# Kernel optimization log

Hardware: AMD Instinct MI355X
Metric: run time of the kernel (lower is better)

## Reference

```python
import jax, jax.numpy as jnp
import numpy as np

NE, NR = 100000, 200
STT, ABS, REL, RDIM = 512, 256, 256, 384
GAMMA = 12.0
PI = 3.141592653589793
EMB_RNG_R = float(np.sqrt(6.0 / (NR + RDIM)))
B = 8192


def setup_inputs() -> dict:
    key = jax.random.key(0)
    ks = jax.random.split(key, 16)
    cols = [
        jax.random.randint(ks[0], (B, 1), 0, NE),      # s
        jax.random.randint(ks[1], (B, 1), 0, NR),      # r
        jax.random.randint(ks[2], (B, 1), 0, NE),      # o
        jax.random.randint(ks[3], (B, 1), 0, 31),      # d
        jax.random.randint(ks[4], (B, 1), 0, 12),      # m
        jax.random.randint(ks[5], (B, 1), 0, 100),     # y
        jax.random.randint(ks[6], (B, 2 * NR), 0, 1000),  # context times
    ]
    x = jnp.concatenate(cols, axis=1).astype(jnp.int64)
    s = 0.02
    return {
        "x": x,
        "e_emb": jax.random.normal(ks[7], (NE, STT), jnp.float32) * s,
        "r_emb": jax.random.normal(ks[8], (NR, RDIM), jnp.float32) * s,
        "d_frq": jax.random.normal(ks[9], (NE, ABS), jnp.float32) * s,
        "d_phi": jax.random.normal(ks[10], (NE, ABS), jnp.float32) * s,
        "d_amp": jax.random.normal(ks[11], (NE, ABS // 2), jnp.float32) * s,
        "m_frq": jax.random.normal(ks[12], (NE, ABS), jnp.float32) * s,
        "m_phi": jax.random.normal(ks[13], (NE, ABS), jnp.float32) * s,
        "m_amp": jax.random.normal(ks[14], (NE, ABS // 2), jnp.float32) * s,
        "w_e": jax.random.normal(ks[15], (STT, REL // 2), jnp.float32) * s,
        "w_rp": jax.random.normal(jax.random.fold_in(key, 99), (NR, NR, 1), jnp.float32) * s,
    }


def _pos_emb(t):  # t: float [N] -> [N, REL]
    f = 1.0 / (10000.0 ** (jnp.arange(0, REL, 2, dtype=jnp.float32) / REL))
    rs = t[:, None] * f[None, :]
    return jnp.concatenate([jnp.cos(rs), jnp.sin(rs)], axis=1)


def reference(x, e_emb, r_emb, d_frq, d_phi, d_amp, m_frq, m_phi, m_amp, w_e, w_rp):
    f32 = jnp.float32

    def t_emb(e, d, m):  # e int [B], d,m float [B,1] -> [B, ABS]
        re_d, im_d = jnp.split(d * d_frq[e] + d_phi[e], 2, axis=1)
        ad = d_amp[e]
        demb = jnp.concatenate([ad * jnp.cos(re_d), ad * jnp.sin(im_d)], axis=1)
        re_m, im_m = jnp.split(m * m_frq[e] + m_phi[e], 2, axis=1)
        am = m_amp[e]
        memb = jnp.concatenate([am * jnp.cos(re_m), am * jnp.sin(im_m)], axis=1)
        return demb + memb

    def e_p_emb(e):  # e: [B,1,STT] -> [B,1,REL]
        re_w, im_w = jnp.split(w_e, 2, axis=0)
        re_e, im_e = jnp.split(e, 2, axis=2)
        re_p = re_e @ re_w - im_e @ im_w
        im_p = im_e @ re_w - re_e @ im_w  # note: minus, matching source
        return jnp.concatenate([re_p, im_p], axis=2)

    def e_r_emb(r_idx, e_t):  # e_t: [B,NR] float -> [B,REL,1]
        er = _pos_emb(e_t.reshape(-1)).reshape(e_t.shape[0], NR, REL)
        er = jnp.transpose(er, (0, 2, 1))  # [B,REL,NR]
        return jnp.einsum('bdn,bno->bdo', er, w_rp[r_idx])

    s_idx, r_idx, o_idx = x[:, 0], x[:, 1], x[:, 2]
    d_abs = x[:, 3:4].astype(f32)
    m_abs = x[:, 4:5].astype(f32)
    c_s = x[:, -2 * NR:-NR].astype(f32)
    c_o = x[:, -NR:].astype(f32)

    s = e_emb[s_idx][:, None, :]
    s_t = t_emb(s_idx, d_abs, m_abs)[:, None, :]
    s_p = e_p_emb(s)
    s_r = e_r_emb(r_idx, c_s)

    o = e_emb[o_idx][:, None, :]
    o_t = t_emb(o_idx, d_abs, m_abs)[:, None, :]
    o_p = e_p_emb(o)
    o_r = e_r_emb(r_idx, c_o)

    r = r_emb[r_idx][:, None, :]  # [B,1,RDIM]
    p_r = r / (EMB_RNG_R / PI)
    re_r, im_r = jnp.cos(p_r), jnp.sin(p_r)

    re_s, im_s = jnp.split(s, 2, axis=2)
    re_st, im_st = jnp.split(s_t, 2, axis=2)
    re_s = jnp.concatenate([re_s, re_st], axis=2)  # [B,1,RDIM]
    im_s = jnp.concatenate([im_s, im_st], axis=2)
    re_o, im_o = jnp.split(o, 2, axis=2)
    re_ot, im_ot = jnp.split(o_t, 2, axis=2)
    re_o = jnp.concatenate([re_o, re_ot], axis=2)
    im_o = jnp.concatenate([im_o, im_ot], axis=2)

    # RotatE complex rotation score on static+absolute part
    re_sc = re_s * re_r - im_s * im_r - re_o
    im_sc = re_s * im_r + im_s * re_r - im_o
    sc_abs = jnp.sqrt(re_sc * re_sc + im_sc * im_sc).sum(axis=2)

    # relative-time score from projected embeddings + relation-context embeddings
    s_rel = s_p + jnp.transpose(s_r, (0, 2, 1))  # [B,1,REL]
    o_rel = o_p + jnp.transpose(o_r, (0, 2, 1))
    re_sr, im_sr = jnp.split(s_rel, 2, axis=2)
    re_or, im_or = jnp.split(o_rel, 2, axis=2)
    dre, dim = re_sr - re_or, im_sr - im_or
    sc_rel = jnp.sqrt(dre * dre + dim * dim).sum(axis=2)

    return GAMMA - (sc_abs + sc_rel)  # [B,1]
```

## Files before the change

### kernel.cpp

```cpp
#include <hip/hip_runtime.h>
#include <cstdint>

#define B_ROWS 8192
#define XSTR   406
#define GAMMA_C 12.0f
#define SCALE_ANG 30.994217f

#define KH     1024
#define HPAD   1028

#define NT_BLK 128
#define NW_BLK 64
#define NF_BLK 512
#define NS_BLK 4096
#define NMRG   (NF_BLK + NS_BLK)

#define TF_BYTES    (KH*256*2)
#define WCAT_BYTES  (512*256*2)
#define WS_FULL     ((size_t)(TF_BYTES + WCAT_BYTES))
#define OLDTAB_BYTES (1000*256*2)
#define WS_OLD       ((size_t)(OLDTAB_BYTES + WCAT_BYTES))

typedef __attribute__((ext_vector_type(8))) short short8v;
typedef __attribute__((ext_vector_type(4))) float float4v;

__device__ __forceinline__ float bfLo(uint32_t u) { return __uint_as_float(u << 16); }
__device__ __forceinline__ float bfHi(uint32_t u) { return __uint_as_float(u & 0xffff0000u); }
__device__ __forceinline__ float bf1(unsigned short u) { return __uint_as_float((uint32_t)u << 16); }

__device__ __forceinline__ uint32_t f2bf_u(float x) {
  uint32_t u = __float_as_uint(x);
  u += 0x7fffu + ((u >> 16) & 1u);
  return u >> 16;
}
__device__ __forceinline__ unsigned short f2bf(float x) { return (unsigned short)f2bf_u(x); }

__device__ __forceinline__ short8v cvt8(float4 a, float4 b) {
  short8v r;
  r[0] = (short)f2bf(a.x); r[1] = (short)f2bf(a.y);
  r[2] = (short)f2bf(a.z); r[3] = (short)f2bf(a.w);
  r[4] = (short)f2bf(b.x); r[5] = (short)f2bf(b.y);
  r[6] = (short)f2bf(b.z); r[7] = (short)f2bf(b.w);
  return r;
}

__global__ __launch_bounds__(256) void kge_prep0(
    const float* __restrict__ w_e,
    unsigned short* __restrict__ tf, unsigned short* __restrict__ wcat) {
  const int bid = blockIdx.x;
  const int tid = threadIdx.x;
  const int sub = tid >> 6, l = tid & 63;
  if (bid < NT_BLK) {
    const int fragid = bid * 4 + sub;
    const int kt = fragid >> 4, nt = fragid & 15;
    const int c = nt * 16 + (l & 15);
    const float f = exp2f(-(float)(c & 127) * (13.287712379549449f / 128.f));
    __align__(16) unsigned short v[8];
    #pragma unroll
    for (int jj = 0; jj < 8; ++jj) {
      int k = kt * 32 + ((l >> 4) << 3) + jj;
      float val = 0.f;
      if (k < 1000) {
        float s, cv;
        sincosf((float)k * f, &s, &cv);
        val = (c < 128) ? cv : s;
      }
      v[jj] = f2bf(val);
    }
    ((uint4*)tf)[fragid * 64 + l] = *(const uint4*)v;
  } else {
    const int fragid = (bid - NT_BLK) * 4 + sub;
    const int kk = fragid >> 4, nt = fragid & 15;
    const int c = nt * 16 + (l & 15);
    __align__(16) unsigned short v[8];
    #pragma unroll
    for (int jj = 0; jj < 8; ++jj) {
      int k = kk * 32 + ((l >> 4) << 3) + jj;
      float s = (k < 256) ? 1.f : -1.f;
      float val = (c < 128) ? s * w_e[k * 128 + c]
                            : -s * w_e[(k ^ 256) * 128 + (c - 128)];
      v[jj] = f2bf(val);
    }
    ((uint4*)wcat)[fragid * 64 + l] = *(const uint4*)v;
  }
}

__global__ __launch_bounds__(256) void kge_merged(
    const int* __restrict__ x, const float* __restrict__ e_emb,
    const float* __restrict__ r_emb,
    const float* __restrict__ d_frq, const float* __restrict__ d_phi, const float* __restrict__ d_amp,
    const float* __restrict__ m_frq, const float* __restrict__ m_phi, const float* __restrict__ m_amp,
    const float* __restrict__ w_rp,
    const unsigned short* __restrict__ wcat, const unsigned short* __restrict__ tf,
    float* __restrict__ out) {
  __shared__ __align__(16) float lds_f[16 * HPAD];
  __shared__ float st2[2][2][256];
  __shared__ float redl[4];
  __shared__ float prel[4][16];
  const int tid = threadIdx.x;
  const int w = tid >> 6, l = tid & 63;

  if (blockIdx.x < NF_BLK) {
    const int m0 = blockIdx.x * 16;

    #pragma unroll
    for (int i = tid; i < 16 * HPAD / 4; i += 256)
      ((float4*)lds_f)[i] = (float4){0, 0, 0, 0};
    __syncthreads();

    {
      const int hr = tid >> 4, sub16 = tid & 15;
      const int row = m0 + hr;
      const int* xr = x + (size_t)row * XSTR;
      const int rid = xr[1];
      const int* cp = xr + 6;
      const float* wp = w_rp + (size_t)rid * 200;
      float* hrow = lds_f + hr * HPAD;
      for (int n = sub16; n < 200; n += 16) {
        float wv = wp[n];
        atomicAdd(&hrow[cp[n]], wv);
        atomicAdd(&hrow[cp[200 + n]], -wv);
      }
    }

    const int rowA = m0 + (l & 15);
    const int* xrA = x + (size_t)rowA * XSTR;
    const float* Esp = e_emb + (size_t)xrA[0] * 512 + ((l >> 4) << 3);
    const float* Eop = e_emb + (size_t)xrA[2] * 512 + ((l >> 4) << 3);
    const short8v* wq = (const short8v*)wcat;
    const short8v* tq = (const short8v*)tf;

    float4v acc[16];
    #pragma unroll
    for (int i = 0; i < 16; ++i) acc[i] = (float4v){0, 0, 0, 0};

    #pragma unroll
    for (int kt = 4 * w; kt < 4 * w + 4; ++kt) {
      float4 s0 = *(const float4*)(Esp + kt * 32);
      float4 s1 = *(const float4*)(Esp + kt * 32 + 4);
      float4 o0 = *(const float4*)(Eop + kt * 32);
      float4 o1 = *(const float4*)(Eop + kt * 32 + 4);
      float4 d0 = {s0.x - o0.x, s0.y - o0.y, s0.z - o0.z, s0.w - o0.w};
      float4 d1 = {s1.x - o1.x, s1.y - o1.y, s1.z - o1.z, s1.w - o1.w};
      short8v a = cvt8(d0, d1);
      const short8v* bsrc = wq + (size_t)kt * 1024;
      #pragma unroll
      for (int nt = 0; nt < 16; ++nt)
        acc[nt] = __builtin_amdgcn_mfma_f32_16x16x32_bf16(a, bsrc[nt * 64 + l], acc[nt], 0, 0, 0);
    }
    __syncthreads();

    {
      const float* hbase = lds_f + (l & 15) * HPAD + ((l >> 4) << 3);
      #pragma unroll
      for (int g = 8 * w; g < 8 * w + 8; ++g) {
        float4 h0 = *(const float4*)(hbase + g * 32);
        float4 h1 = *(const float4*)(hbase + g * 32 + 4);
        short8v a = cvt8(h0, h1);
        const short8v* bsrc = tq + (size_t)g * 1024;
        #pragma unroll
        for (int nt = 0; nt < 16; ++nt)
          acc[nt] = __builtin_amdgcn_mfma_f32_16x16x32_bf16(a, bsrc[nt * 64 + l], acc[nt], 0, 0, 0);
      }
    }
    __syncthreads();

    float* part = lds_f;
    #pragma unroll
    for (int nt = 0; nt < 16; ++nt)
      #pragma unroll
      for (int q = 0; q < 4; ++q)
        part[((w * 16 + nt) * 256) + q * 64 + l] = acc[nt][q];
    __syncthreads();

    {
      float sq[4] = {0.f, 0.f, 0.f, 0.f};
      #pragma unroll
      for (int pp = 0; pp < 2; ++pp) {
        const int p = 2 * w + pp;
        #pragma unroll
        for (int q = 0; q < 4; ++q) {
          const int idx = q * 64 + l;
          float dre = part[(0 * 16 + p) * 256 + idx] + part[(1 * 16 + p) * 256 + idx]
                    + part[(2 * 16 + p) * 256 + idx] + part[(3 * 16 + p) * 256 + idx];
          float dim = part[(0 * 16 + p + 8) * 256 + idx] + part[(1 * 16 + p + 8) * 256 + idx]
                    + part[(2 * 16 + p + 8) * 256 + idx] + part[(3 * 16 + p + 8) * 256 + idx];
          sq[q] += sqrtf(dre * dre + dim * dim);
        }
      }
      #pragma unroll
      for (int q = 0; q < 4; ++q) {
        float s = sq[q];
        s += __shfl_xor(s, 1); s += __shfl_xor(s, 2);
        s += __shfl_xor(s, 4); s += __shfl_xor(s, 8);
        if ((l & 15) == 0) prel[w][(l >> 4) * 4 + q] = s;
      }
    }
    __syncthreads();
    if (tid < 16) {
      const int r = tid;
      float srel = prel[0][r] + prel[1][r] + prel[2][r] + prel[3][r];
      atomicAdd(&out[m0 + r], -srel);
    }
  } else {
    const int bid = blockIdx.x - NF_BLK;
    const int rsub = tid >> 7;
    const int row = bid * 2 + rsub;
    const int j = tid & 127;
    const int* xr = x + (size_t)row * XSTR;
    const int eS = xr[0], rid = xr[1], eO = xr[2];
    const float dv = (float)xr[3], mv = (float)xr[4];
    const int j2 = 2 * j;
    #pragma unroll
    for (int ent = 0; ent < 2; ++ent) {
      const int e = ent ? eO : eS;
      float2 fd = *(const float2*)&d_frq[(size_t)e * 256 + j2];
      float2 pd = *(const float2*)&d_phi[(size_t)e * 256 + j2];
      float2 fm = *(const float2*)&m_frq[(size_t)e * 256 + j2];
      float2 pm = *(const float2*)&m_phi[(size_t)e * 256 + j2];
      const int ja = j2 & 127;
      float2 ad = *(const float2*)&d_amp[(size_t)e * 128 + ja];
      float2 am = *(const float2*)&m_amp[(size_t)e * 128 + ja];
      float a0 = fmaf(dv, fd.x, pd.x), a1 = fmaf(dv, fd.y, pd.y);
      float b0 = fmaf(mv, fm.x, pm.x), b1 = fmaf(mv, fm.y, pm.y);
      float t0, t1, u0, u1;
      if (j2 < 128) { t0 = __cosf(a0); t1 = __cosf(a1); u0 = __cosf(b0); u1 = __cosf(b1); }
      else          { t0 = __sinf(a0); t1 = __sinf(a1); u0 = __sinf(b0); u1 = __sinf(b1); }
      st2[rsub][ent][j2]     = fmaf(ad.x, t0, am.x * u0);
      st2[rsub][ent][j2 + 1] = fmaf(ad.y, t1, am.y * u1);
    }
    __syncthreads();
    const float* Es = e_emb + (size_t)eS * 512;
    const float* Eo = e_emb + (size_t)eO * 512;
    const float* Rr = r_emb + (size_t)rid * 384;
    float sabs = 0.f;
    #pragma unroll
    for (int t3 = 0; t3 < 3; ++t3) {
      const int u = t3 * 128 + j;
      float ang = Rr[u] * SCALE_ANG;
      float sr = __sinf(ang), cr = __cosf(ang);
      float res, ims, reo, imo;
      if (t3 < 2) {
        res = Es[u]; ims = Es[256 + u];
        reo = Eo[u]; imo = Eo[256 + u];
      } else {
        res = st2[rsub][0][j]; ims = st2[rsub][0][128 + j];
        reo = st2[rsub][1][j]; imo = st2[rsub][1][128 + j];
      }
      float rsc = res * cr - ims * sr - reo;
      float isc = res * sr + ims * cr - imo;
      sabs += sqrtf(rsc * rsc + isc * isc);
    }
    #pragma unroll
    for (int off = 32; off > 0; off >>= 1) sabs += __shfl_down(sabs, off);
    if (l == 0) redl[w] = sabs;
    __syncthreads();
    if (j == 0) atomicAdd(&out[row], GAMMA_C - (redl[2 * rsub] + redl[2 * rsub + 1]));
  }
}

#define NTH    512
#define RPB    8
#define ERB    (2*RPB)
#define APAD   520

__global__ void kge_table_old(unsigned short* __restrict__ tab) {
  int t = blockIdx.x;
  int j = threadIdx.x;
  double f = pow(10000.0, -(double)j / 128.0);
  double ang = (double)t * f;
  int q = j >> 1, lo = j & 1;
  tab[t * 256 + 4 * q + lo]     = f2bf((float)cos(ang));
  tab[t * 256 + 4 * q + 2 + lo] = f2bf((float)sin(ang));
}

__global__ void kge_wcat_old(const float* __restrict__ w_e, unsigned short* __restrict__ wcat) {
  int bid = blockIdx.x;
  int kk = bid >> 4, nt = bid & 15;
  int l = threadIdx.x;
  __align__(16) unsigned short v[8];
  int c = nt * 16 + (l & 15);
  #pragma unroll
  for (int j = 0; j < 8; ++j) {
    int k = kk * 32 + ((l >> 4) << 3) + j;
    float s = (k < 256) ? 1.f : -1.f;
    float val = (c < 128) ? s * w_e[k * 128 + c]
                          : -s * w_e[(k ^ 256) * 128 + (c - 128)];
    v[j] = f2bf(val);
  }
  ((uint4*)wcat)[bid * 64 + l] = *(const uint4*)v;
}

__global__ __launch_bounds__(NTH, 4) void kge_main3(
    const int* __restrict__ x,
    const float* __restrict__ e_emb, const float* __restrict__ r_emb,
    const float* __restrict__ d_frq, const float* __restrict__ d_phi, const float* __restrict__ d_amp,
    const float* __restrict__ m_frq, const float* __restrict__ m_phi, const float* __restrict__ m_amp,
    const float* __restrict__ w_rp,
    const unsigned short* __restrict__ tab, const unsigned short* __restrict__ wcat,
    float* __restrict__ out) {
  __shared__ __align__(16) unsigned short A[ERB][APAD];
  __shared__ __align__(16) unsigned short stb[ERB][256];
  __shared__ __align__(16) float p[ERB][256];
  __shared__ int meta[RPB][6];

  const int tid = threadIdx.x;
  const int base_row = blockIdx.x * RPB;
  const int w = tid >> 6, l = tid & 63;

  if (tid < RPB * 6) {
    int r = tid / 6, f = tid % 6;
    meta[r][f] = x[(size_t)(base_row + r) * XSTR + f];
  }
  __syncthreads();

  for (int i = tid; i < ERB * 128; i += NTH) {
    int er = i >> 7, k4 = i & 127;
    int e = (er & 1) ? meta[er >> 1][2] : meta[er >> 1][0];
    float4 v = ((const float4*)e_emb)[(size_t)e * 128 + k4];
    uint2 pk;
    pk.x = f2bf_u(v.x) | (f2bf_u(v.y) << 16);
    pk.y = f2bf_u(v.z) | (f2bf_u(v.w) << 16);
    *(uint2*)&A[er][k4 * 4] = pk;
  }
  for (int it = tid; it < ERB * 256; it += NTH) {
    int j = it & 255, er = it >> 8, r = er >> 1;
    int e = (er & 1) ? meta[r][2] : meta[r][0];
    float dv = (float)meta[r][3], mv = (float)meta[r][4];
    size_t b256 = (size_t)e * 256 + j, b128 = (size_t)e * 128 + (j & 127);
    float argd = fmaf(dv, d_frq[b256], d_phi[b256]);
    float argm = fmaf(mv, m_frq[b256], m_phi[b256]);
    float vd = (j < 128) ? d_amp[b128] * __cosf(argd) : d_amp[b128] * __sinf(argd);
    float vm = (j < 128) ? m_amp[b128] * __cosf(argm) : m_amp[b128] * __sinf(argm);
    stb[er][j] = f2bf(vd + vm);
  }

  float s0 = 0, s1 = 0, s2 = 0, s3 = 0, o0 = 0, o1 = 0, o2 = 0, o3 = 0;
  {
    const int wu  = __builtin_amdgcn_readfirstlane(w);
    const int rid = __builtin_amdgcn_readfirstlane(meta[wu][1]);
    const int*   cp = x + (size_t)(base_row + wu) * XSTR + 6;
    const float* wp = w_rp + (size_t)rid * 200;
    const uint2* tl = ((const uint2*)tab) + l;
    #pragma unroll 2
    for (int n = 0; n < 200; ++n) {
      float wv = wp[n];
      int cS = cp[n];
      int cO = cp[200 + n];
      uint2 qs = tl[(size_t)cS * 64];
      uint2 qo = tl[(size_t)cO * 64];
      s0 = fmaf(wv, bfLo(qs.x), s0); s1 = fmaf(wv, bfHi(qs.x), s1);
      s2 = fmaf(wv, bfLo(qs.y), s2); s3 = fmaf(wv, bfHi(qs.y), s3);
      o0 = fmaf(wv, bfLo(qo.x), o0); o1 = fmaf(wv, bfHi(qo.x), o1);
      o2 = fmaf(wv, bfLo(qo.y), o2); o3 = fmaf(wv, bfHi(qo.y), o3);
    }
  }
  __syncthreads();

  {
    float4v acc0 = {0, 0, 0, 0}, acc1 = {0, 0, 0, 0};
    const int nt0 = 2 * w, nt1 = 2 * w + 1;
    const short8v* bp = (const short8v*)wcat;
    const unsigned short* arow = &A[l & 15][(l >> 4) << 3];
    #pragma unroll 8
    for (int kk = 0; kk < 16; ++kk) {
      short8v a  = *(const short8v*)(arow + kk * 32);
      short8v b0 = bp[(kk * 16 + nt0) * 64 + l];
      short8v b1 = bp[(kk * 16 + nt1) * 64 + l];
      acc0 = __builtin_amdgcn_mfma_f32_16x16x32_bf16(a, b0, acc0, 0, 0, 0);
      acc1 = __builtin_amdgcn_mfma_f32_16x16x32_bf16(a, b1, acc1, 0, 0, 0);
    }
    int col = l & 15, rbase = (l >> 4) * 4;
    #pragma unroll
    for (int q = 0; q < 4; ++q) {
      p[rbase + q][nt0 * 16 + col] = acc0[q];
      p[rbase + q][nt1 * 16 + col] = acc1[q];
    }
  }
  __syncthreads();

  {
    int es = 2 * w, eo = 2 * w + 1;
    p[es][2 * l] += s0; p[es][2 * l + 1] += s1;
    p[es][128 + 2 * l] += s2; p[es][129 + 2 * l] += s3;
    p[eo][2 * l] += o0; p[eo][2 * l + 1] += o1;
    p[eo][128 + 2 * l] += o2; p[eo][129 + 2 * l] += o3;
  }
  __syncthreads();

  {
    int r = w;
    int rid = meta[r][1];
    float sabs = 0.f;
    #pragma unroll
    for (int u0 = 0; u0 < 384; u0 += 64) {
      int u = u0 + l;
      float ang = r_emb[(size_t)rid * 384 + u] * SCALE_ANG;
      float sr = __sinf(ang), cr = __cosf(ang);
      float res, ims, reo, imo;
      if (u < 256) {
        res = bf1(A[2 * r][u]);       ims = bf1(A[2 * r][256 + u]);
        reo = bf1(A[2 * r + 1][u]);   imo = bf1(A[2 * r + 1][256 + u]);
      } else {
        int uu = u - 256;
        res = bf1(stb[2 * r][uu]);     ims = bf1(stb[2 * r][128 + uu]);
        reo = bf1(stb[2 * r + 1][uu]); imo = bf1(stb[2 * r + 1][128 + uu]);
      }
      float rsc = res * cr - ims * sr - reo;
      float isc = res * sr + ims * cr - imo;
      sabs += sqrtf(rsc * rsc + isc * isc);
    }
    float srel = 0.f;
    #pragma unroll
    for (int u0 = 0; u0 < 128; u0 += 64) {
      int u = u0 + l;
      float dre = p[2 * r][u] - p[2 * r + 1][u];
      float dim = p[2 * r][128 + u] - p[2 * r + 1][128 + u];
      srel += sqrtf(dre * dre + dim * dim);
    }
    float tot = sabs + srel;
    #pragma unroll
    for (int off = 32; off > 0; off >>= 1) tot += __shfl_down(tot, off);
    if (l == 0) out[base_row + r] = GAMMA_C - tot;
  }
}

extern "C" void kernel_launch(void* const* d_in, const int* in_sizes, int n_in,
                              void* d_out, int out_size, void* d_ws, size_t ws_size,
                              hipStream_t stream) {
  (void)in_sizes; (void)n_in; (void)out_size;
  const int*   x     = (const int*)d_in[0];
  const float* e_emb = (const float*)d_in[1];
  const float* r_emb = (const float*)d_in[2];
  const float* d_frq = (const float*)d_in[3];
  const float* d_phi = (const float*)d_in[4];
  const float* d_amp = (const float*)d_in[5];
  const float* m_frq = (const float*)d_in[6];
  const float* m_phi = (const float*)d_in[7];
  const float* m_amp = (const float*)d_in[8];
  const float* w_e   = (const float*)d_in[9];
  const float* w_rp  = (const float*)d_in[10];
  float* out = (float*)d_out;

  if (ws_size >= WS_FULL) {
    char* base = (char*)d_ws;
    unsigned short* tf   = (unsigned short*)base;
    unsigned short* wcat = (unsigned short*)(base + TF_BYTES);
    hipMemsetAsync(out, 0, (size_t)B_ROWS * sizeof(float), stream);
    kge_prep0<<<dim3(NT_BLK + NW_BLK), dim3(256), 0, stream>>>(w_e, tf, wcat);
    kge_merged<<<dim3(NMRG), dim3(256), 0, stream>>>(
        x, e_emb, r_emb, d_frq, d_phi, d_amp, m_frq, m_phi, m_amp, w_rp,
        wcat, tf, out);
  } else if (ws_size >= WS_OLD) {
    unsigned short* tab  = (unsigned short*)d_ws;
    unsigned short* wcat = (unsigned short*)((char*)d_ws + OLDTAB_BYTES);
    kge_table_old<<<dim3(1000), dim3(128), 0, stream>>>(tab);
    kge_wcat_old<<<dim3(256), dim3(64), 0, stream>>>(w_e, wcat);
    kge_main3<<<dim3(B_ROWS / RPB), dim3(NTH), 0, stream>>>(
        x, e_emb, r_emb, d_frq, d_phi, d_amp, m_frq, m_phi, m_amp, w_rp,
        tab, wcat, out);
  }
}
```

Baseline: 70.48 us.

## Precompute bf16 relation-context histograms in prep kernel and rebalance MFMA work

Builds the per-row relation-context scatter histogram in the prep kernel and writes it to a bf16 global buffer of 8192x1024. The main kernel then loads histogram fragments directly instead of zeroing and atomically filling a large LDS tile. Each block now handles 32 rows with two wave pairs that split the K range unevenly, and partial sums are combined through a smaller LDS buffer. This cuts LDS use and raises occupancy, at the cost of about 16 MB of extra global writes and reads plus a larger workspace requirement. If the workspace is too small, it falls back to the older path.

```diff
diff --git a/kernel.cpp b/kernel.cpp
--- a/kernel.cpp
+++ b/kernel.cpp
@@ -7,17 +7,20 @@
 #define SCALE_ANG 30.994217f
 
 #define KH     1024
-#define HPAD   1028
 
 #define NT_BLK 128
 #define NW_BLK 64
-#define NF_BLK 512
+#define NG_BLK 2048
+#define NPREP  (NT_BLK + NW_BLK + NG_BLK)
+
+#define NF_BLK 256
 #define NS_BLK 4096
 #define NMRG   (NF_BLK + NS_BLK)
 
 #define TF_BYTES    (KH*256*2)
 #define WCAT_BYTES  (512*256*2)
-#define WS_FULL     ((size_t)(TF_BYTES + WCAT_BYTES))
+#define G_BYTES     (8192*KH*2)
+#define WS_FULL     ((size_t)(TF_BYTES + WCAT_BYTES + G_BYTES))
 #define OLDTAB_BYTES (1000*256*2)
 #define WS_OLD       ((size_t)(OLDTAB_BYTES + WCAT_BYTES))
 
@@ -44,12 +47,16 @@
   return r;
 }
 
-__global__ __launch_bounds__(256) void kge_prep0(
+__global__ __launch_bounds__(256) void kge_prepG(
+    const int* __restrict__ x, const float* __restrict__ w_rp,
     const float* __restrict__ w_e,
-    unsigned short* __restrict__ tf, unsigned short* __restrict__ wcat) {
+    unsigned short* __restrict__ tf, unsigned short* __restrict__ wcat,
+    unsigned short* __restrict__ G) {
+  __shared__ float Hl[4][KH];
   const int bid = blockIdx.x;
   const int tid = threadIdx.x;
   const int sub = tid >> 6, l = tid & 63;
+
   if (bid < NT_BLK) {
     const int fragid = bid * 4 + sub;
     const int kt = fragid >> 4, nt = fragid & 15;
@@ -68,7 +75,7 @@
       v[jj] = f2bf(val);
     }
     ((uint4*)tf)[fragid * 64 + l] = *(const uint4*)v;
-  } else {
+  } else if (bid < NT_BLK + NW_BLK) {
     const int fragid = (bid - NT_BLK) * 4 + sub;
     const int kk = fragid >> 4, nt = fragid & 15;
     const int c = nt * 16 + (l & 15);
@@ -82,51 +89,47 @@
       v[jj] = f2bf(val);
     }
     ((uint4*)wcat)[fragid * 64 + l] = *(const uint4*)v;
-  }
-}
-
-__global__ __launch_bounds__(256) void kge_merged(
+  } else {
+    const int row = (bid - NT_BLK - NW_BLK) * 4 + sub;
+    float4 z = {0, 0, 0, 0};
+    for (int i = l; i < KH / 4; i += 64) ((float4*)Hl[sub])[i] = z;
+    const int rid = x[(size_t)row * XSTR + 1];
+    const int* cp = x + (size_t)row * XSTR + 6;
+    const float* wp = w_rp + (size_t)rid * 200;
+    for (int n = l; n < 200; n += 64) {
+      float wv = wp[n];
+      atomicAdd(&Hl[sub][cp[n]], wv);
+      atomicAdd(&Hl[sub][cp[200 + n]], -wv);
+    }
+    unsigned short* dst = G + (size_t)row * KH;
+    for (int i = l; i < KH / 2; i += 64) {
+      float a = Hl[sub][2 * i], b = Hl[sub][2 * i + 1];
+      ((uint32_t*)dst)[i] = f2bf_u(a) | (f2bf_u(b) << 16);
+    }
+  }
+}
+
+__global__ __launch_bounds__(256) void kge_merged2(
     const int* __restrict__ x, const float* __restrict__ e_emb,
     const float* __restrict__ r_emb,
     const float* __restrict__ d_frq, const float* __restrict__ d_phi, const float* __restrict__ d_amp,
     const float* __restrict__ m_frq, const float* __restrict__ m_phi, const float* __restrict__ m_amp,
-    const float* __restrict__ w_rp,
+    const unsigned short* __restrict__ G,
     const unsigned short* __restrict__ wcat, const unsigned short* __restrict__ tf,
     float* __restrict__ out) {
-  __shared__ __align__(16) float lds_f[16 * HPAD];
-  __shared__ float st2[2][2][256];
+  __shared__ __align__(16) float shbuf[2 * 16 * 256];
+  __shared__ float srl[32];
   __shared__ float redl[4];
-  __shared__ float prel[4][16];
   const int tid = threadIdx.x;
   const int w = tid >> 6, l = tid & 63;
 
   if (blockIdx.x < NF_BLK) {
-    const int m0 = blockIdx.x * 16;
-
-    #pragma unroll
-    for (int i = tid; i < 16 * HPAD / 4; i += 256)
-      ((float4*)lds_f)[i] = (float4){0, 0, 0, 0};
-    __syncthreads();
-
-    {
-      const int hr = tid >> 4, sub16 = tid & 15;
-      const int row = m0 + hr;
-      const int* xr = x + (size_t)row * XSTR;
-      const int rid = xr[1];
-      const int* cp = xr + 6;
-      const float* wp = w_rp + (size_t)rid * 200;
-      float* hrow = lds_f + hr * HPAD;
-      for (int n = sub16; n < 200; n += 16) {
-        float wv = wp[n];
-        atomicAdd(&hrow[cp[n]], wv);
-        atomicAdd(&hrow[cp[200 + n]], -wv);
-      }
-    }
-
-    const int rowA = m0 + (l & 15);
-    const int* xrA = x + (size_t)rowA * XSTR;
-    const float* Esp = e_emb + (size_t)xrA[0] * 512 + ((l >> 4) << 3);
-    const float* Eop = e_emb + (size_t)xrA[2] * 512 + ((l >> 4) << 3);
+    const int m0 = blockIdx.x * 32;
+    const int pair = w >> 1, kh = w & 1;
+    const int mrow = m0 + pair * 16;
+
+    const int rowA = mrow + (l & 15);
+    const unsigned short* Gp = G + (size_t)rowA * KH + ((l >> 4) << 3);
     const short8v* wq = (const short8v*)wcat;
     const short8v* tq = (const short8v*)tf;
 
@@ -134,75 +137,69 @@
     #pragma unroll
     for (int i = 0; i < 16; ++i) acc[i] = (float4v){0, 0, 0, 0};
 
-    #pragma unroll
-    for (int kt = 4 * w; kt < 4 * w + 4; ++kt) {
-      float4 s0 = *(const float4*)(Esp + kt * 32);
-      float4 s1 = *(const float4*)(Esp + kt * 32 + 4);
-      float4 o0 = *(const float4*)(Eop + kt * 32);
-      float4 o1 = *(const float4*)(Eop + kt * 32 + 4);
-      float4 d0 = {s0.x - o0.x, s0.y - o0.y, s0.z - o0.z, s0.w - o0.w};
-      float4 d1 = {s1.x - o1.x, s1.y - o1.y, s1.z - o1.z, s1.w - o1.w};
-      short8v a = cvt8(d0, d1);
-      const short8v* bsrc = wq + (size_t)kt * 1024;
-      #pragma unroll
-      for (int nt = 0; nt < 16; ++nt)
-        acc[nt] = __builtin_amdgcn_mfma_f32_16x16x32_bf16(a, bsrc[nt * 64 + l], acc[nt], 0, 0, 0);
-    }
-    __syncthreads();
-
-    {
-      const float* hbase = lds_f + (l & 15) * HPAD + ((l >> 4) << 3);
-      #pragma unroll
-      for (int g = 8 * w; g < 8 * w + 8; ++g) {
-        float4 h0 = *(const float4*)(hbase + g * 32);
-        float4 h1 = *(const float4*)(hbase + g * 32 + 4);
-        short8v a = cvt8(h0, h1);
+    if (kh == 0) {
+      const int* xrA = x + (size_t)rowA * XSTR;
+      const float* Esp = e_emb + (size_t)xrA[0] * 512 + ((l >> 4) << 3);
+      const float* Eop = e_emb + (size_t)xrA[2] * 512 + ((l >> 4) << 3);
+      #pragma unroll 2
+      for (int kt = 0; kt < 16; ++kt) {
+        float4 s0 = *(const float4*)(Esp + kt * 32);
+        float4 s1 = *(const float4*)(Esp + kt * 32 + 4);
+        float4 o0 = *(const float4*)(Eop + kt * 32);
+        float4 o1 = *(const float4*)(Eop + kt * 32 + 4);
+        float4 d0 = {s0.x - o0.x, s0.y - o0.y, s0.z - o0.z, s0.w - o0.w};
+        float4 d1 = {s1.x - o1.x, s1.y - o1.y, s1.z - o1.z, s1.w - o1.w};
+        short8v a = cvt8(d0, d1);
+        const short8v* bsrc = wq + (size_t)kt * 1024;
+        #pragma unroll
+        for (int nt = 0; nt < 16; ++nt)
+          acc[nt] = __builtin_amdgcn_mfma_f32_16x16x32_bf16(a, bsrc[nt * 64 + l], acc[nt], 0, 0, 0);
+      }
+      #pragma unroll 2
+      for (int g = 0; g < 8; ++g) {
+        short8v a = *(const short8v*)(Gp + g * 32);
         const short8v* bsrc = tq + (size_t)g * 1024;
         #pragma unroll
         for (int nt = 0; nt < 16; ++nt)
           acc[nt] = __builtin_amdgcn_mfma_f32_16x16x32_bf16(a, bsrc[nt * 64 + l], acc[nt], 0, 0, 0);
       }
+    } else {
+      #pragma unroll 2
+      for (int g = 8; g < 32; ++g) {
+        short8v a = *(const short8v*)(Gp + g * 32);
+        const short8v* bsrc = tq + (size_t)g * 1024;
+        #pragma unroll
+        for (int nt = 0; nt < 16; ++nt)
+          acc[nt] = __builtin_amdgcn_mfma_f32_16x16x32_bf16(a, bsrc[nt * 64 + l], acc[nt], 0, 0, 0);
+      }
+      #pragma unroll
+      for (int nt = 0; nt < 16; ++nt)
+        #pragma unroll
+        for (int q = 0; q < 4; ++q)
+          shbuf[(pair * 16 + nt) * 256 + q * 64 + l] = acc[nt][q];
     }
     __syncthreads();
 
-    float* part = lds_f;
-    #pragma unroll
-    for (int nt = 0; nt < 16; ++nt)
-      #pragma unroll
-      for (int q = 0; q < 4; ++q)
-        part[((w * 16 + nt) * 256) + q * 64 + l] = acc[nt][q];
-    __syncthreads();
-
-    {
-      float sq[4] = {0.f, 0.f, 0.f, 0.f};
-      #pragma unroll
-      for (int pp = 0; pp < 2; ++pp) {
-        const int p = 2 * w + pp;
-        #pragma unroll
-        for (int q = 0; q < 4; ++q) {
-          const int idx = q * 64 + l;
-          float dre = part[(0 * 16 + p) * 256 + idx] + part[(1 * 16 + p) * 256 + idx]
-                    + part[(2 * 16 + p) * 256 + idx] + part[(3 * 16 + p) * 256 + idx];
-          float dim = part[(0 * 16 + p + 8) * 256 + idx] + part[(1 * 16 + p + 8) * 256 + idx]
-                    + part[(2 * 16 + p + 8) * 256 + idx] + part[(3 * 16 + p + 8) * 256 + idx];
-          sq[q] += sqrtf(dre * dre + dim * dim);
-        }
-      }
+    if (kh == 0) {
       #pragma unroll
       for (int q = 0; q < 4; ++q) {
-        float s = sq[q];
+        float s = 0.f;
+        #pragma unroll
+        for (int nt = 0; nt < 8; ++nt) {
+          const int idx = q * 64 + l;
+          float dre = acc[nt][q]     + shbuf[(pair * 16 + nt) * 256 + idx];
+          float dim = acc[nt + 8][q] + shbuf[(pair * 16 + nt + 8) * 256 + idx];
+          s += sqrtf(dre * dre + dim * dim);
+        }
         s += __shfl_xor(s, 1); s += __shfl_xor(s, 2);
         s += __shfl_xor(s, 4); s += __shfl_xor(s, 8);
-        if ((l & 15) == 0) prel[w][(l >> 4) * 4 + q] = s;
+        if ((l & 15) == 0) srl[pair * 16 + (l >> 4) * 4 + q] = s;
       }
     }
     __syncthreads();
-    if (tid < 16) {
-      const int r = tid;
-      float srel = prel[0][r] + prel[1][r] + prel[2][r] + prel[3][r];
-      atomicAdd(&out[m0 + r], -srel);
-    }
+    if (tid < 32) atomicAdd(&out[m0 + tid], -srl[tid]);
   } else {
+    float (*st2)[2][256] = (float(*)[2][256])shbuf;
     const int bid = blockIdx.x - NF_BLK;
     const int rsub = tid >> 7;
     const int row = bid * 2 + rsub;
@@ -446,11 +443,12 @@
     char* base = (char*)d_ws;
     unsigned short* tf   = (unsigned short*)base;
     unsigned short* wcat = (unsigned short*)(base + TF_BYTES);
+    unsigned short* G    = (unsigned short*)(base + TF_BYTES + WCAT_BYTES);
     hipMemsetAsync(out, 0, (size_t)B_ROWS * sizeof(float), stream);
-    kge_prep0<<<dim3(NT_BLK + NW_BLK), dim3(256), 0, stream>>>(w_e, tf, wcat);
-    kge_merged<<<dim3(NMRG), dim3(256), 0, stream>>>(
-        x, e_emb, r_emb, d_frq, d_phi, d_amp, m_frq, m_phi, m_amp, w_rp,
-        wcat, tf, out);
+    kge_prepG<<<dim3(NPREP), dim3(256), 0, stream>>>(x, w_rp, w_e, tf, wcat, G);
+    kge_merged2<<<dim3(NMRG), dim3(256), 0, stream>>>(
+        x, e_emb, r_emb, d_frq, d_phi, d_amp, m_frq, m_phi, m_amp,
+        G, wcat, tf, out);
   } else if (ws_size >= WS_OLD) {
     unsigned short* tab  = (unsigned short*)d_ws;
     unsigned short* wcat = (unsigned short*)((char*)d_ws + OLDTAB_BYTES);
```

Result: slower. 91.34 us (+29.6%).
